# Optimization experiments

Measured on AMD Instinct MI355X. Metric: run time of the kernel, lower is better.

Reference implementation:

```python
import jax, jax.numpy as jnp
import numpy as np

N_STREAMS = 4096


def setup_inputs() -> dict:
    key = jax.random.key(0)
    # Plain Gaussian (well-separated singular values; the polar factor math is
    # identical to the module's eye + 0.01*randn init, just a different point).
    H_raw = jax.random.normal(key, (N_STREAMS, N_STREAMS), dtype=jnp.float32)
    return {"H_raw": H_raw}


def reference(H_raw) -> jnp.ndarray:
    # OrthogonalMixing.forward: orthogonal polar factor of H_raw via thin SVD.
    U, s, Vh = jnp.linalg.svd(H_raw, full_matrices=False)
    return U @ Vh  # (s, s), satisfies H^T H = I
```

## Files before the change

kernel.cpp:

```cpp
#include <hip/hip_runtime.h>
#include <hip/hip_bf16.h>
#include <hip/hip_fp16.h>

#define NN 4096
#define NGROW 8
#define NPOL 2
#define NITER (NGROW + NPOL)
#define NPOW 12
#define NTRI 528
#define PRESCALE 32.0f

using f16 = _Float16;
typedef __attribute__((ext_vector_type(4))) float f32x4;
typedef __attribute__((ext_vector_type(8))) f16 h16x8;

__device__ inline void gl_lds16(const void* g, void* l) {
  __builtin_amdgcn_global_load_lds(
      (const __attribute__((address_space(1))) unsigned int*)(unsigned long long)(uintptr_t)g,
      (__attribute__((address_space(3))) unsigned int*)(uintptr_t)l,
      16, 0, 0);
}

template <int EPI, int TRI>
__global__ __launch_bounds__(256, 4) void gemm_nt(
    const f16* __restrict__ P, const f16* __restrict__ Q,
    void* __restrict__ Out, const f16* __restrict__ aux,
    float alpha, float beta) {
  int bi, bj;
  if (TRI) {
    const int t = blockIdx.x;
    int r = (int)((sqrtf(8.0f * (float)t + 1.0f) - 1.0f) * 0.5f);
    while ((r + 1) * (r + 2) / 2 <= t) ++r;
    while (r * (r + 1) / 2 > t) --r;
    bi = r;
    bj = t - r * (r + 1) / 2;
  } else {
    bi = blockIdx.x;
    bj = blockIdx.y;
  }

  __shared__ f16 lp[128 * 64];
  __shared__ f16 lq[128 * 64];

  const int tid = threadIdx.x;
  const int lane = tid & 63;
  const int wv = tid >> 6;
  const int wr = wv >> 1, wc = wv & 1;

  const int m = lane & 15;
  const int qd = lane >> 4;
  const int lrow = lane >> 3;
  const int lchunk = lane & 7;

  f32x4 acc[4][4] = {};

  for (int k0 = 0; k0 < NN; k0 += 64) {
    __syncthreads();
#pragma unroll
    for (int s = 0; s < 4; ++s) {
      const int t = wv * 4 + s;
      const int r = t * 8 + lrow;
      const int gc = lchunk ^ (r & 7);
      const f16* gp = P + (size_t)(bi * 128 + r) * NN + k0 + gc * 8;
      gl_lds16(gp, &lp[t * 512 + lane * 8]);
      const f16* gq = Q + (size_t)(bj * 128 + r) * NN + k0 + gc * 8;
      gl_lds16(gq, &lq[t * 512 + lane * 8]);
    }
    __syncthreads();

#pragma unroll
    for (int sub = 0; sub < 2; ++sub) {
      h16x8 av[4], bv[4];
#pragma unroll
      for (int f = 0; f < 4; ++f) {
        const int ra = wr * 64 + f * 16 + m;
        const int ca = (sub * 4 + qd) ^ (ra & 7);
        av[f] = *(const h16x8*)&lp[ra * 64 + ca * 8];
        const int rb = wc * 64 + f * 16 + m;
        const int cb = (sub * 4 + qd) ^ (rb & 7);
        bv[f] = *(const h16x8*)&lq[rb * 64 + cb * 8];
      }
#pragma unroll
      for (int fr = 0; fr < 4; ++fr)
#pragma unroll
        for (int fc = 0; fc < 4; ++fc)
          acc[fr][fc] = __builtin_amdgcn_mfma_f32_16x16x32_f16(
              av[fr], bv[fc], acc[fr][fc], 0, 0, 0);
    }
  }

#pragma unroll
  for (int fr = 0; fr < 4; ++fr) {
#pragma unroll
    for (int fc = 0; fc < 4; ++fc) {
#pragma unroll
      for (int rg = 0; rg < 4; ++rg) {
        const int lr = wr * 64 + fr * 16 + qd * 4 + rg;
        const int lc = wc * 64 + fc * 16 + m;
        const size_t idx = (size_t)(bi * 128 + lr) * NN + bj * 128 + lc;
        float v = beta * acc[fr][fc][rg];
        if (alpha != 0.0f) v += alpha * (float)aux[idx];
        if (EPI == 0)
          ((f16*)Out)[idx] = (f16)v;
        else
          ((float*)Out)[idx] = v;
        if (TRI && bi != bj) {
          const size_t idxT = (size_t)(bj * 128 + lc) * NN + bi * 128 + lr;
          ((f16*)Out)[idxT] = (f16)v;
        }
      }
    }
  }
}

__global__ void transpose_h(const unsigned short* __restrict__ in,
                            unsigned short* __restrict__ out) {
  __shared__ unsigned short tile[64][65];
  const int tx = threadIdx.x & 63;
  const int ty = threadIdx.x >> 6;
  const int bx = blockIdx.x, by = blockIdx.y;
#pragma unroll
  for (int rr = 0; rr < 16; ++rr) {
    const int row = rr * 4 + ty;
    tile[row][tx] = in[(size_t)(by * 64 + row) * NN + bx * 64 + tx];
  }
  __syncthreads();
#pragma unroll
  for (int rr = 0; rr < 16; ++rr) {
    const int row = rr * 4 + ty;
    out[(size_t)(bx * 64 + row) * NN + by * 64 + tx] = tile[tx][row];
  }
}

__global__ __launch_bounds__(256) void powmv(const f16* __restrict__ A,
                                             const float* __restrict__ vin,
                                             const float* __restrict__ snin,
                                             float* __restrict__ vout,
                                             float* __restrict__ snout) {
  const float scale = rsqrtf(*snin);
  const int row = blockIdx.x * 4 + (threadIdx.x >> 6);
  const int lane = threadIdx.x & 63;
  const f16* arow = A + (size_t)row * NN;
  float acc = 0.0f;
#pragma unroll
  for (int p = 0; p < 8; ++p) {
    const int c = p * 512 + lane * 8;
    const h16x8 av = *(const h16x8*)(arow + c);
    const float4 w0 = *(const float4*)(vin + c);
    const float4 w1 = *(const float4*)(vin + c + 4);
    acc += (float)av[0] * w0.x + (float)av[1] * w0.y + (float)av[2] * w0.z +
           (float)av[3] * w0.w + (float)av[4] * w1.x + (float)av[5] * w1.y +
           (float)av[6] * w1.z + (float)av[7] * w1.w;
  }
  for (int off = 32; off; off >>= 1) acc += __shfl_down(acc, off, 64);
  if (lane == 0) {
    const float u = acc * scale;
    vout[row] = u;
    atomicAdd(snout, u * u);
  }
}

__global__ void init_pw(float* __restrict__ v0, float* __restrict__ slots) {
  const int t = threadIdx.x;
  if (t < 64) slots[t] = (t == 1) ? 1.0f : 0.0f;
  for (int i = t; i < NN; i += 256) {
    const unsigned h = (unsigned)i * 2654435761u;
    v0[i] = ((h >> 16) & 1) ? 0.015625f : -0.015625f;
  }
}

__global__ void reduce_sumsq(const float* __restrict__ h, float* __restrict__ slots) {
  float acc = 0.0f;
  const size_t total = (size_t)NN * NN;
  for (size_t i = (size_t)blockIdx.x * blockDim.x + threadIdx.x; i < total;
       i += (size_t)gridDim.x * blockDim.x) {
    const float v = h[i];
    acc += v * v;
  }
  for (int off = 32; off; off >>= 1) acc += __shfl_down(acc, off, 64);
  __shared__ float ws[4];
  const int lane = threadIdx.x & 63, wv = threadIdx.x >> 6;
  if (lane == 0) ws[wv] = acc;
  __syncthreads();
  if (threadIdx.x == 0) atomicAdd(&slots[0], ws[0] + ws[1] + ws[2] + ws[3]);
}

__global__ void scale_cast(const float* __restrict__ h, const float* __restrict__ slots,
                           f16* __restrict__ xb, int mode) {
  float inv = rsqrtf(slots[0]) * PRESCALE;
  if (mode) inv *= rsqrtf(1.10f * sqrtf(slots[1 + NPOW]));
  const size_t i = ((size_t)blockIdx.x * blockDim.x + threadIdx.x) * 4;
  const float4 v = *(const float4*)(h + i);
  union { f16 hh[4]; ushort4 u; } cvt;
  cvt.hh[0] = (f16)(v.x * inv);
  cvt.hh[1] = (f16)(v.y * inv);
  cvt.hh[2] = (f16)(v.z * inv);
  cvt.hh[3] = (f16)(v.w * inv);
  *(ushort4*)(xb + i) = cvt.u;
}

__global__ void rescale_f16(f16* __restrict__ a, const float* __restrict__ slots) {
  const float cA = 1.0f / (1.10f * sqrtf(slots[1 + NPOW]));
  const size_t i = ((size_t)blockIdx.x * 256 + threadIdx.x) * 8;
  h16x8 v = *(h16x8*)(a + i);
  h16x8 o;
#pragma unroll
  for (int j = 0; j < 8; ++j) o[j] = (f16)((float)v[j] * cA);
  *(h16x8*)(a + i) = o;
}

extern "C" void kernel_launch(void* const* d_in, const int* in_sizes, int n_in,
                              void* d_out, int out_size, void* d_ws, size_t ws_size,
                              hipStream_t stream) {
  (void)in_sizes; (void)n_in; (void)out_size; (void)ws_size;
  const float* H = (const float*)d_in[0];
  float* out = (float*)d_out;
  char* ws = (char*)d_ws;

  f16* P0 = (f16*)ws;
  f16* P1 = (f16*)(ws + ((size_t)32 << 20));
  f16* Ab = (f16*)(ws + ((size_t)64 << 20));
  f16* Bb = (f16*)((char*)d_out + ((size_t)32 << 20));
  float* v0 = (float*)d_out;
  float* v1 = (float*)((char*)d_out + 16384);
  float* slots = (float*)((char*)d_out + 32768);

  const dim3 gfull(32, 32), tb(256), gt(64, 64);

  init_pw<<<1, 256, 0, stream>>>(v0, slots);
  reduce_sumsq<<<1024, 256, 0, stream>>>(H, slots);
  scale_cast<<<(NN * (size_t)NN) / 4 / 256, 256, 0, stream>>>(H, slots, P0, 0);
  transpose_h<<<gt, tb, 0, stream>>>((const unsigned short*)P0, (unsigned short*)P1);
  gemm_nt<0, 1><<<NTRI, tb, 0, stream>>>(P1, P1, Ab, (f16*)nullptr, 0.0f, 1.0f);
  for (int k = 0; k < NPOW; ++k) {
    const float* vi = (k & 1) ? v1 : v0;
    float* vo = (k & 1) ? v0 : v1;
    powmv<<<1024, 256, 0, stream>>>(Ab, vi, &slots[1 + k], vo, &slots[2 + k]);
  }
  rescale_f16<<<(NN * (size_t)NN) / 8 / 256, 256, 0, stream>>>(Ab, slots);
  scale_cast<<<(NN * (size_t)NN) / 4 / 256, 256, 0, stream>>>(H, slots, P0, 1);

  f16* X = P0;
  f16* Y = P1;
  const float GA = 3.4445f, GB = -4.7750f, GC = 2.0315f;
  const float PA = 1.875f, PB = -1.25f, PC = 0.375f;

  for (int it = 0; it < NITER; ++it) {
    const bool polish = it >= NGROW;
    const bool last = (it == NITER - 1);
    const float qa = polish ? PA : GA, qb = polish ? PB : GB, qc = polish ? PC : GC;

    if (it > 0) {
      transpose_h<<<gt, tb, 0, stream>>>((const unsigned short*)X, (unsigned short*)Y);
      gemm_nt<0, 1><<<NTRI, tb, 0, stream>>>(Y, Y, Ab, (f16*)nullptr, 0.0f, 1.0f);
    }
    f16* Bdst = last ? Y : Bb;
    gemm_nt<0, 1><<<NTRI, tb, 0, stream>>>(Ab, Ab, Bdst, Ab, qb, qc);
    if (!last) {
      gemm_nt<0, 0><<<gfull, tb, 0, stream>>>(X, Bdst, Y, X, qa, 1.0f);
      f16* t = X; X = Y; Y = t;
    } else {
      gemm_nt<1, 0><<<gfull, tb, 0, stream>>>(X, Bdst, out, X, qa, 1.0f);
    }
  }
}
```

Baseline: 4.586 ms.

## Split-K the symmetric triangular GEMMs and combine halves in a separate kernel

The triangular (symmetric) GEMMs launched only 528 blocks. They now run as a 2-way split-K grid. The first K-half writes fp32 partials to a scratch buffer and the second writes fp16 into the destination. A new combine_tri kernel adds the two halves, applies the alpha/beta epilogue and writes the mirrored transpose through LDS, so the GEMM no longer does scattered transposed stores. The goal is better CU occupancy on the large GPU. The cost is extra launches and extra partial-buffer traffic, plus a loss of precision because the second half is rounded to fp16. Buffers are reshuffled so the output is used as fp32 scratch.

After: 4.667 ms. No clear change (+1.8%).

```diff
diff --git a/kernel.cpp b/kernel.cpp
--- a/kernel.cpp
+++ b/kernel.cpp
@@ -8,6 +8,7 @@
 #define NITER (NGROW + NPOL)
 #define NPOW 12
 #define NTRI 528
+#define KHALF 2048
 #define PRESCALE 32.0f
 
 using f16 = _Float16;
@@ -21,22 +22,29 @@
       16, 0, 0);
 }
 
-template <int EPI, int TRI>
+__device__ inline void tri_decode(int t, int& bi, int& bj) {
+  int r = (int)((sqrtf(8.0f * (float)t + 1.0f) - 1.0f) * 0.5f);
+  while ((r + 1) * (r + 2) / 2 <= t) ++r;
+  while (r * (r + 1) / 2 > t) --r;
+  bi = r;
+  bj = t - r * (r + 1) / 2;
+}
+
+template <int MODE>
 __global__ __launch_bounds__(256, 4) void gemm_nt(
     const f16* __restrict__ P, const f16* __restrict__ Q,
     void* __restrict__ Out, const f16* __restrict__ aux,
-    float alpha, float beta) {
-  int bi, bj;
-  if (TRI) {
-    const int t = blockIdx.x;
-    int r = (int)((sqrtf(8.0f * (float)t + 1.0f) - 1.0f) * 0.5f);
-    while ((r + 1) * (r + 2) / 2 <= t) ++r;
-    while (r * (r + 1) / 2 > t) --r;
-    bi = r;
-    bj = t - r * (r + 1) / 2;
+    float alpha, float beta, float* __restrict__ p0) {
+  int bi, bj, kbeg, kend;
+  if (MODE == 2) {
+    tri_decode(blockIdx.x, bi, bj);
+    kbeg = blockIdx.y * KHALF;
+    kend = kbeg + KHALF;
   } else {
     bi = blockIdx.x;
     bj = blockIdx.y;
+    kbeg = 0;
+    kend = NN;
   }
 
   __shared__ f16 lp[128 * 64];
@@ -54,7 +62,7 @@
 
   f32x4 acc[4][4] = {};
 
-  for (int k0 = 0; k0 < NN; k0 += 64) {
+  for (int k0 = kbeg; k0 < kend; k0 += 64) {
     __syncthreads();
 #pragma unroll
     for (int s = 0; s < 4; ++s) {
@@ -97,20 +105,89 @@
       for (int rg = 0; rg < 4; ++rg) {
         const int lr = wr * 64 + fr * 16 + qd * 4 + rg;
         const int lc = wc * 64 + fc * 16 + m;
-        const size_t idx = (size_t)(bi * 128 + lr) * NN + bj * 128 + lc;
-        float v = beta * acc[fr][fc][rg];
-        if (alpha != 0.0f) v += alpha * (float)aux[idx];
-        if (EPI == 0)
-          ((f16*)Out)[idx] = (f16)v;
-        else
-          ((float*)Out)[idx] = v;
-        if (TRI && bi != bj) {
-          const size_t idxT = (size_t)(bj * 128 + lc) * NN + bi * 128 + lr;
-          ((f16*)Out)[idxT] = (f16)v;
+        if (MODE == 2) {
+          if (blockIdx.y == 0)
+            p0[(size_t)blockIdx.x * 16384 + lr * 128 + lc] = acc[fr][fc][rg];
+          else
+            ((f16*)Out)[(size_t)(bi * 128 + lr) * NN + bj * 128 + lc] =
+                (f16)acc[fr][fc][rg];
+        } else {
+          const size_t idx = (size_t)(bi * 128 + lr) * NN + bj * 128 + lc;
+          float v = beta * acc[fr][fc][rg];
+          if (alpha != 0.0f) v += alpha * (float)aux[idx];
+          if (MODE == 0)
+            ((f16*)Out)[idx] = (f16)v;
+          else
+            ((float*)Out)[idx] = v;
         }
       }
     }
   }
+}
+
+__global__ __launch_bounds__(256) void combine_tri(
+    const float* __restrict__ p0, f16* __restrict__ dest,
+    const f16* __restrict__ aux, float alpha, float beta) {
+  int bi, bj;
+  tri_decode(blockIdx.x, bi, bj);
+  __shared__ f16 tile[64][72];
+  const int rr = threadIdx.x >> 2;
+  const int cg = (threadIdx.x & 3) * 16;
+
+#pragma unroll
+  for (int qr = 0; qr < 2; ++qr)
+#pragma unroll
+    for (int qc = 0; qc < 2; ++qc) {
+      const int grow = bi * 128 + qr * 64 + rr;
+      const size_t gidx = (size_t)grow * NN + bj * 128 + qc * 64 + cg;
+      const size_t pidx = (size_t)blockIdx.x * 16384 + (qr * 64 + rr) * 128 + qc * 64 + cg;
+      const float4 a0 = *(const float4*)(p0 + pidx);
+      const float4 a1 = *(const float4*)(p0 + pidx + 4);
+      const float4 a2 = *(const float4*)(p0 + pidx + 8);
+      const float4 a3 = *(const float4*)(p0 + pidx + 12);
+      const h16x8 b0 = *(const h16x8*)(dest + gidx);
+      const h16x8 b1 = *(const h16x8*)(dest + gidx + 8);
+      float v[16] = {a0.x, a0.y, a0.z, a0.w, a1.x, a1.y, a1.z, a1.w,
+                     a2.x, a2.y, a2.z, a2.w, a3.x, a3.y, a3.z, a3.w};
+#pragma unroll
+      for (int j = 0; j < 8; ++j) {
+        v[j] = beta * (v[j] + (float)b0[j]);
+        v[j + 8] = beta * (v[j + 8] + (float)b1[j]);
+      }
+      if (alpha != 0.0f) {
+        const h16x8 x0 = *(const h16x8*)(aux + gidx);
+        const h16x8 x1 = *(const h16x8*)(aux + gidx + 8);
+#pragma unroll
+        for (int j = 0; j < 8; ++j) {
+          v[j] += alpha * (float)x0[j];
+          v[j + 8] += alpha * (float)x1[j];
+        }
+      }
+      h16x8 o0, o1;
+#pragma unroll
+      for (int j = 0; j < 8; ++j) { o0[j] = (f16)v[j]; o1[j] = (f16)v[j + 8]; }
+      *(h16x8*)(dest + gidx) = o0;
+      *(h16x8*)(dest + gidx + 8) = o1;
+
+      if (bi != bj) {
+#pragma unroll
+        for (int j = 0; j < 8; ++j) {
+          tile[rr][cg + j] = o0[j];
+          tile[rr][cg + 8 + j] = o1[j];
+        }
+        __syncthreads();
+        h16x8 m0, m1;
+#pragma unroll
+        for (int j = 0; j < 8; ++j) {
+          m0[j] = tile[cg + j][rr];
+          m1[j] = tile[cg + 8 + j][rr];
+        }
+        const size_t tidx = (size_t)(bj * 128 + qc * 64 + rr) * NN + bi * 128 + qr * 64 + cg;
+        *(h16x8*)(dest + tidx) = m0;
+        *(h16x8*)(dest + tidx + 8) = m1;
+        __syncthreads();
+      }
+    }
 }
 
 __global__ void transpose_h(const unsigned short* __restrict__ in,
@@ -220,18 +297,19 @@
   f16* P0 = (f16*)ws;
   f16* P1 = (f16*)(ws + ((size_t)32 << 20));
   f16* Ab = (f16*)(ws + ((size_t)64 << 20));
-  f16* Bb = (f16*)((char*)d_out + ((size_t)32 << 20));
-  float* v0 = (float*)d_out;
-  float* v1 = (float*)((char*)d_out + 16384);
-  float* slots = (float*)((char*)d_out + 32768);
-
-  const dim3 gfull(32, 32), tb(256), gt(64, 64);
+  float* pf = (float*)d_out;
+  float* v0 = (float*)((char*)d_out + ((size_t)60 << 20));
+  float* v1 = v0 + 4096;
+  float* slots = v1 + 4096;
+
+  const dim3 gfull(32, 32), gsplit(NTRI, 2), tb(256), gt(64, 64);
 
   init_pw<<<1, 256, 0, stream>>>(v0, slots);
   reduce_sumsq<<<1024, 256, 0, stream>>>(H, slots);
   scale_cast<<<(NN * (size_t)NN) / 4 / 256, 256, 0, stream>>>(H, slots, P0, 0);
   transpose_h<<<gt, tb, 0, stream>>>((const unsigned short*)P0, (unsigned short*)P1);
-  gemm_nt<0, 1><<<NTRI, tb, 0, stream>>>(P1, P1, Ab, (f16*)nullptr, 0.0f, 1.0f);
+  gemm_nt<2><<<gsplit, tb, 0, stream>>>(P1, P1, Ab, nullptr, 0.0f, 0.0f, pf);
+  combine_tri<<<NTRI, tb, 0, stream>>>(pf, Ab, nullptr, 0.0f, 1.0f);
   for (int k = 0; k < NPOW; ++k) {
     const float* vi = (k & 1) ? v1 : v0;
     float* vo = (k & 1) ? v0 : v1;
@@ -241,7 +319,7 @@
   scale_cast<<<(NN * (size_t)NN) / 4 / 256, 256, 0, stream>>>(H, slots, P0, 1);
 
   f16* X = P0;
-  f16* Y = P1;
+  f16* Aslot = Ab;
   const float GA = 3.4445f, GB = -4.7750f, GC = 2.0315f;
   const float PA = 1.875f, PB = -1.25f, PC = 0.375f;
 
@@ -251,16 +329,17 @@
     const float qa = polish ? PA : GA, qb = polish ? PB : GB, qc = polish ? PC : GC;
 
     if (it > 0) {
-      transpose_h<<<gt, tb, 0, stream>>>((const unsigned short*)X, (unsigned short*)Y);
-      gemm_nt<0, 1><<<NTRI, tb, 0, stream>>>(Y, Y, Ab, (f16*)nullptr, 0.0f, 1.0f);
-    }
-    f16* Bdst = last ? Y : Bb;
-    gemm_nt<0, 1><<<NTRI, tb, 0, stream>>>(Ab, Ab, Bdst, Ab, qb, qc);
+      transpose_h<<<gt, tb, 0, stream>>>((const unsigned short*)X, (unsigned short*)P1);
+      gemm_nt<2><<<gsplit, tb, 0, stream>>>(P1, P1, Aslot, nullptr, 0.0f, 0.0f, pf);
+      combine_tri<<<NTRI, tb, 0, stream>>>(pf, Aslot, nullptr, 0.0f, 1.0f);
+    }
+    gemm_nt<2><<<gsplit, tb, 0, stream>>>(Aslot, Aslot, P1, nullptr, 0.0f, 0.0f, pf);
+    combine_tri<<<NTRI, tb, 0, stream>>>(pf, P1, Aslot, qb, qc);
     if (!last) {
-      gemm_nt<0, 0><<<gfull, tb, 0, stream>>>(X, Bdst, Y, X, qa, 1.0f);
-      f16* t = X; X = Y; Y = t;
+      gemm_nt<0><<<gfull, tb, 0, stream>>>(X, P1, Aslot, X, qa, 1.0f, nullptr);
+      f16* t = X; X = Aslot; Aslot = t;
     } else {
-      gemm_nt<1, 0><<<gfull, tb, 0, stream>>>(X, Bdst, out, X, qa, 1.0f);
-    }
-  }
-}
+      gemm_nt<1><<<gfull, tb, 0, stream>>>(X, P1, out, X, qa, 1.0f, nullptr);
+    }
+  }
+}
```
